# Kernel optimization log

Hardware: AMD Instinct MI355X
Metric: run time of the kernel (lower is better)

Reference implementation:

```python
import jax, jax.numpy as jnp
import numpy as np

# Mamba2 hyperparameters
D_MODEL = 768
D_STATE = 64
D_CONV = 4
EXPAND = 2
HEADDIM = 64
CHUNK = 64
D_INNER = EXPAND * D_MODEL            # 1536
NHEADS = D_INNER // HEADDIM           # 24
D_IN_PROJ = 2 * D_INNER + 2 * D_STATE + NHEADS  # 3224
CONV_DIM = D_INNER + 2 * D_STATE      # 1664
B_SZ = 8
SEQ = 4096  # multiple of CHUNK -> no padding branch


def setup_inputs() -> dict:
    key = jax.random.key(0)
    ks = jax.random.split(key, 6)
    u = jax.random.normal(ks[0], (B_SZ, SEQ, D_MODEL), jnp.float32)
    # fan-in scaled weights (matches nn.Linear/Conv1d default init scale)
    W_in = jax.random.normal(ks[1], (D_IN_PROJ, D_MODEL), jnp.float32) / np.sqrt(D_MODEL).astype(np.float32)
    conv_w = jax.random.normal(ks[2], (CONV_DIM, 1, D_CONV), jnp.float32) / np.sqrt(D_CONV).astype(np.float32)
    conv_b = jnp.zeros((CONV_DIM,), jnp.float32)
    dt_bias = jax.random.uniform(ks[3], (NHEADS,), jnp.float32, -4.0, 1.0)  # nn.init.uniform_(-4, 1)
    A_log = jnp.full((NHEADS,), -np.log(2.0), jnp.float32)                  # nn.init.constant_(-log 2)
    D_param = jnp.ones((NHEADS,), jnp.float32)
    norm_w = jnp.ones((D_INNER,), jnp.float32)
    W_out = jax.random.normal(ks[4], (D_MODEL, D_INNER), jnp.float32) / np.sqrt(D_INNER).astype(np.float32)
    return dict(u=u, W_in=W_in, conv_w=conv_w, conv_b=conv_b, dt_bias=dt_bias,
                A_log=A_log, D_param=D_param, norm_w=norm_w, W_out=W_out)


def _segsum(x):
    """Stable segment sum: out[..., i, j] = sum_{j < k <= i} x[..., k]; -inf above diagonal."""
    T = x.shape[-1]
    lower_strict = jnp.tril(jnp.ones((T, T), bool), -1)
    xe = jnp.where(lower_strict, x[..., :, None], 0.0)   # broadcast x over last (col) axis
    s = jnp.cumsum(xe, axis=-2)
    lower = jnp.tril(jnp.ones((T, T), bool), 0)
    return jnp.where(lower, s, -jnp.inf)


def _ssd(x, A, B, C, chunk):
    """Chunked SSD. x:(b,L,h,p)  A:(b,L,h)  B,C:(b,L,1,n)."""
    b, L, h, p = x.shape
    c = L // chunk
    n = B.shape[-1]
    x = x.reshape(b, c, chunk, h, p)
    A = A.reshape(b, c, chunk, h).transpose(0, 3, 1, 2)   # b h c l
    B = B.reshape(b, c, chunk, 1, n)
    C = C.reshape(b, c, chunk, 1, n)
    A_cs = jnp.cumsum(A, axis=-1)                          # b h c l
    # intra-chunk (diagonal) term
    Lmat = jnp.exp(_segsum(A))                             # b h c l s
    Y_diag = jnp.einsum('bclhn,bcshn,bhcls,bcshp->bclhp', C, B, Lmat, x)
    # per-chunk states
    decay_states = jnp.exp(A_cs[..., -1:] - A_cs)          # b h c l
    states = jnp.einsum('bclhn,bhcl,bclhp->bchpn', B, decay_states, x)
    states = jnp.concatenate([jnp.zeros_like(states[:, :1]), states], axis=1)  # b (c+1) h p n
    # inter-chunk recurrence
    A_last = jnp.pad(A_cs[..., -1], ((0, 0), (0, 0), (1, 0)))  # b h (c+1)
    decay_chunk = jnp.exp(_segsum(A_last))                     # b h (c+1) (c+1)
    new_states = jnp.einsum('bhzc,bchpn->bzhpn', decay_chunk, states)
    states = new_states[:, :-1]                                # b c h p n
    # off-diagonal (state-to-output) term
    Y_off = jnp.einsum('bclhn,bchpn,bhcl->bclhp', C, states, jnp.exp(A_cs))
    return (Y_diag + Y_off).reshape(b, L, h, p)


def reference(u, W_in, conv_w, conv_b, dt_bias, A_log, D_param, norm_w, W_out):
    b, L, _ = u.shape  # L % CHUNK == 0, so pad branch is a no-op
    zxbcdt = u @ W_in.T                                    # (b, L, D_IN_PROJ)
    z = zxbcdt[..., :D_INNER]
    xBC = zxbcdt[..., D_INNER:D_INNER + CONV_DIM]
    dt = jax.nn.softplus(zxbcdt[..., D_INNER + CONV_DIM:] + dt_bias)  # (b, L, h)
    # causal depthwise conv1d (torch pads both sides by d_conv-1 then slices [:L] == left pad)
    xBC = jax.lax.conv_general_dilated(
        xBC.transpose(0, 2, 1), conv_w, window_strides=(1,),
        padding=[(D_CONV - 1, 0)], dimension_numbers=('NCH', 'OIH', 'NCH'),
        feature_group_count=CONV_DIM)
    xBC = jax.nn.silu(xBC.transpose(0, 2, 1) + conv_b)     # (b, L, CONV_DIM)
    x = xBC[..., :D_INNER].reshape(b, L, NHEADS, HEADDIM)
    Bm = xBC[..., D_INNER:D_INNER + D_STATE][:, :, None, :]  # (b, L, 1, n)
    Cm = xBC[..., D_INNER + D_STATE:][:, :, None, :]
    A = -jnp.exp(A_log)                                    # (h,)
    Y = _ssd(x * dt[..., None], A * dt, Bm, Cm, CHUNK)
    y = Y + x * D_param[:, None]                           # skip term
    y = y.reshape(b, L, D_INNER)
    # gated RMSNorm: x * silu(z), then rmsnorm * weight
    y = y * jax.nn.silu(z)
    y = y * jax.lax.rsqrt(jnp.mean(y * y, axis=-1, keepdims=True) + 1e-5) * norm_w
    return y @ W_out.T
```

## Files before the change

### kernel.cpp

```cpp
#include <hip/hip_runtime.h>
#include <stdint.h>

typedef unsigned short u16;
typedef __bf16 bf16x8 __attribute__((ext_vector_type(8)));
typedef float f32x4 __attribute__((ext_vector_type(4)));
typedef unsigned short u16x8 __attribute__((ext_vector_type(8)));
typedef unsigned short u16x4 __attribute__((ext_vector_type(4)));
typedef __attribute__((address_space(1))) unsigned int gu32;
typedef __attribute__((address_space(3))) unsigned int lu32;

__device__ __forceinline__ float bf2f(u16 u){ unsigned int v=((unsigned int)u)<<16; float f; __builtin_memcpy(&f,&v,4); return f; }
__device__ __forceinline__ u16 f2bf(float f){ unsigned int v; __builtin_memcpy(&v,&f,4); v += 0x7fffu + ((v>>16)&1u); return (u16)(v>>16); }
__device__ __forceinline__ int swz(int r,int c){ return (r<<6) + (c ^ ((r&7)<<3)); }
__device__ __forceinline__ void glds16(const void* g, void* l){
  __builtin_amdgcn_global_load_lds((gu32*)g, (lu32*)l, 16, 0, 0);
}

__global__ __launch_bounds__(256) void k_cast(const float* __restrict__ in, u16* __restrict__ out, int n4){
  int i = blockIdx.x*256 + threadIdx.x;
  if (i >= n4) return;
  const f32x4 v = *(const f32x4*)(in + (size_t)i*4);
  u16x4 o; o.x=f2bf(v.x); o.y=f2bf(v.y); o.z=f2bf(v.z); o.w=f2bf(v.w);
  *(u16x4*)(out + (size_t)i*4) = o;
}

__global__ __launch_bounds__(256) void k_cast_pad(const float* __restrict__ in, u16* __restrict__ out){
  int i = blockIdx.x*256 + threadIdx.x;
  int e0 = i*4;
  int row = e0 / 768;
  int col = e0 - row*768;
  u16x4 o;
  if (row < 3224){
    const f32x4 v = *(const f32x4*)(in + (size_t)row*768 + col);
    o.x=f2bf(v.x); o.y=f2bf(v.y); o.z=f2bf(v.z); o.w=f2bf(v.w);
  } else { o.x=0; o.y=0; o.z=0; o.w=0; }
  *(u16x4*)(out + e0) = o;
}

template<int K, int NT, int EPI>
__global__ __launch_bounds__(256,4) void k_gemm(
    const u16* __restrict__ A, const u16* __restrict__ Bw,
    u16* __restrict__ o_z, u16* __restrict__ o_xbc, float* __restrict__ o_dt,
    const float* __restrict__ dt_bias, float* __restrict__ o_f32)
{
  __shared__ __align__(16) u16 Alds[8192];
  __shared__ __align__(16) u16 Blds[8192];
  const int tid = threadIdx.x;
  const int wave = tid>>6, lane = tid&63;
  const int nwg = gridDim.x;
  const int cpx = nwg>>3;
  const int bid = (int)blockIdx.x;
  const int sb  = (bid&7)*cpx + (bid>>3);
  const int m0 = (sb/NT)<<7, n0 = (sb%NT)<<7;
  const int wr = (wave>>1)<<6, wc = (wave&1)<<6;
  const int srow = tid>>3, sc0 = (tid&7)<<3;
  const int lo16 = lane&15, hi = lane>>4;
  f32x4 acc[4][4] = {};
  for (int k0 = 0; k0 < K; k0 += 64){
    #pragma unroll
    for (int i = 0; i < 4; ++i){
      const int row = (i<<5) + srow;
      const int scol = sc0 ^ ((row&7)<<3);
      glds16(A  + (size_t)(m0+row)*K + k0 + scol, &Alds[(i<<11) + (wave<<9)]);
      glds16(Bw + (size_t)(n0+row)*K + k0 + scol, &Blds[(i<<11) + (wave<<9)]);
    }
    __syncthreads();
    #pragma unroll
    for (int kk = 0; kk < 2; ++kk){
      const int kb = (kk<<5) + (hi<<3);
      bf16x8 af[4], bfv[4];
      #pragma unroll
      for (int m = 0; m < 4; ++m){
        const int r = wr + (m<<4) + lo16;
        af[m] = *(const bf16x8*)&Alds[(r<<6) + (kb ^ ((r&7)<<3))];
      }
      #pragma unroll
      for (int n = 0; n < 4; ++n){
        const int r = wc + (n<<4) + lo16;
        bfv[n] = *(const bf16x8*)&Blds[(r<<6) + (kb ^ ((r&7)<<3))];
      }
      #pragma unroll
      for (int m = 0; m < 4; ++m)
      #pragma unroll
      for (int n = 0; n < 4; ++n)
        acc[m][n] = __builtin_amdgcn_mfma_f32_16x16x32_bf16(af[m], bfv[n], acc[m][n], 0,0,0);
    }
    __syncthreads();
  }
  #pragma unroll
  for (int m = 0; m < 4; ++m)
  #pragma unroll
  for (int n = 0; n < 4; ++n)
  #pragma unroll
  for (int i = 0; i < 4; ++i){
    const int gr = m0 + wr + (m<<4) + (hi<<2) + i;
    const int gc = n0 + wc + (n<<4) + lo16;
    const float v = acc[m][n][i];
    if constexpr (EPI == 0){
      if (gc < 1536)      o_z[(size_t)gr*1536 + gc] = f2bf(v);
      else if (gc < 3200) o_xbc[(size_t)gr*1664 + (gc-1536)] = f2bf(v);
      else if (gc < 3224){
        const float t = v + dt_bias[gc-3200];
        o_dt[(size_t)(gc-3200)*32768 + gr] = (t > 20.f) ? t : log1pf(__expf(t));
      }
    } else {
      o_f32[(size_t)gr*768 + gc] = v;
    }
  }
}

__global__ __launch_bounds__(256) void k_conv(
    const u16* __restrict__ xbc, const float* __restrict__ cw, const float* __restrict__ cb,
    const float* __restrict__ dtT,
    u16* __restrict__ xT, u16* __restrict__ Bn, u16* __restrict__ BT, u16* __restrict__ Cn)
{
  const int idx = blockIdx.x*256 + threadIdx.x;
  if (idx >= 4096*208) return;
  const int g  = idx % 208;
  const int pt = idx / 208;
  const int ch0 = g << 3;
  const int m0 = pt << 3;
  const int l0 = m0 & 4095;
  float wgt[8][4], bias8[8];
  #pragma unroll
  for (int j = 0; j < 8; ++j){
    const f32x4 wv = *(const f32x4*)(cw + (size_t)(ch0+j)*4);
    wgt[j][0]=wv.x; wgt[j][1]=wv.y; wgt[j][2]=wv.z; wgt[j][3]=wv.w;
    bias8[j] = cb[ch0+j];
  }
  float acc[8][8];
  #pragma unroll
  for (int p = 0; p < 8; ++p)
  #pragma unroll
  for (int j = 0; j < 8; ++j) acc[p][j] = bias8[j];
  #pragma unroll
  for (int r = -3; r < 8; ++r){
    const int ls = l0 + r;
    if (ls < 0) continue;
    const u16x8 v = *(const u16x8*)(xbc + (size_t)(m0+r)*1664 + ch0);
    float xf[8];
    #pragma unroll
    for (int j = 0; j < 8; ++j) xf[j] = bf2f(v[j]);
    #pragma unroll
    for (int t = 0; t < 4; ++t){
      const int p = r + 3 - t;
      if (p < 0 || p > 7) continue;
      #pragma unroll
      for (int j = 0; j < 8; ++j) acc[p][j] += xf[j] * wgt[j][t];
    }
  }
  #pragma unroll
  for (int p = 0; p < 8; ++p)
  #pragma unroll
  for (int j = 0; j < 8; ++j){ const float s = acc[p][j]; acc[p][j] = s / (1.f + __expf(-s)); }

  const int b = m0 >> 12;
  const int cch = l0 >> 6;
  const int lr0 = l0 & 63;
  if (ch0 < 1536){
    const int h = ch0 >> 6, p0 = ch0 & 63;
    const f32x4 d0 = *(const f32x4*)(dtT + (size_t)h*32768 + m0);
    const f32x4 d1 = *(const f32x4*)(dtT + (size_t)h*32768 + m0 + 4);
    const float dtl[8] = {d0.x,d0.y,d0.z,d0.w,d1.x,d1.y,d1.z,d1.w};
    const size_t rb = (size_t)(b*24+h)*64;
    #pragma unroll
    for (int j = 0; j < 8; ++j){
      const int row = p0 + j;
      u16x8 o;
      #pragma unroll
      for (int p = 0; p < 8; ++p) o[p] = f2bf(acc[p][j] * dtl[p]);
      *(u16x8*)(xT + (rb + row)*4096 + (size_t)cch*64 + (lr0 ^ ((row&7)<<3))) = o;
    }
  } else if (ch0 < 1600){
    const int n0 = ch0 - 1536;
    const size_t tb = ((size_t)(b*64 + cch))*4096;
    #pragma unroll
    for (int p = 0; p < 8; ++p){
      const int lr = lr0 + p;
      u16x8 o;
      #pragma unroll
      for (int j = 0; j < 8; ++j) o[j] = f2bf(acc[p][j]);
      *(u16x8*)(Bn + tb + lr*64 + (n0 ^ ((lr&7)<<3))) = o;
    }
    #pragma unroll
    for (int j = 0; j < 8; ++j){
      const int row = n0 + j;
      u16x8 o;
      #pragma unroll
      for (int p = 0; p < 8; ++p) o[p] = f2bf(acc[p][j]);
      *(u16x8*)(BT + tb + row*64 + (lr0 ^ ((row&7)<<3))) = o;
    }
  } else {
    const int n0 = ch0 - 1600;
    const size_t tb = ((size_t)(b*64 + cch))*4096;
    #pragma unroll
    for (int p = 0; p < 8; ++p){
      const int lr = lr0 + p;
      u16x8 o;
      #pragma unroll
      for (int j = 0; j < 8; ++j) o[j] = f2bf(acc[p][j]);
      *(u16x8*)(Cn + tb + lr*64 + (n0 ^ ((lr&7)<<3))) = o;
    }
  }
}

__global__ __launch_bounds__(256,1) void k_ssd(
    const u16* __restrict__ xT, const u16* __restrict__ Bn, const u16* __restrict__ BT,
    const u16* __restrict__ Cn, const float* __restrict__ dtT, const float* __restrict__ A_log,
    const float* __restrict__ Dp, u16* __restrict__ yo)
{
  __shared__ __align__(16) u16 tiles[2][4][4096];
  __shared__ __align__(16) u16 Ml[4096];
  __shared__ __align__(16) u16 Sbf[4096];
  const int tid = threadIdx.x, wave = tid>>6, lane = tid&63;
  const int lo16 = lane&15, hi = lane>>4;
  const int w16 = wave<<4, hi4 = hi<<2;
  const int b = blockIdx.x / 24, h = blockIdx.x % 24;
  const float Ah = -__expf(A_log[h]);
  const float Dh = Dp[h];
  for (int i = tid; i < 4096; i += 256) Sbf[i] = 0;
  f32x4 Sreg[4] = {};
  const size_t xTg  = (size_t)(b*24+h)*64*4096;
  const size_t bcg  = (size_t)b*64*4096;
  const size_t dtg0 = (size_t)h*32768 + (size_t)b*4096;
  const size_t yb   = (size_t)b*4096*1536 + (size_t)h*64;

  auto stage = [&](int buf, int c){
    u16* dst = &tiles[buf][wave][0];
    if (wave == 0){
      const u16* g0 = xT + xTg + (size_t)c*64 + (size_t)(lane>>3)*4096 + (lane&7)*8;
      #pragma unroll
      for (int s = 0; s < 8; ++s) glds16(g0 + (size_t)s*32768, dst + s*512);
    } else {
      const u16* src = (wave==1 ? Bn : wave==2 ? BT : Cn) + bcg + (size_t)c*4096 + lane*8;
      #pragma unroll
      for (int s = 0; s < 8; ++s) glds16(src + s*512, dst + s*512);
    }
  };

  float dtc = dtT[dtg0 + lane];
  stage(0, 0);

  for (int c = 0; c < 64; ++c){
    float s = Ah * dtc;
    #pragma unroll
    for (int o = 1; o < 64; o <<= 1){ const float t = __shfl_up(s, o); if (lane >= o) s += t; }
    const float Alast = __shfl(s, 63);
    const float lam  = __expf(Alast);
    const float decl = __expf(Alast - s);
    const float elv  = __expf(s);
    float dtn = 0.f;
    if (c < 63){
      dtn = dtT[dtg0 + (size_t)(c+1)*64 + lane];
      stage((c+1)&1, c+1);
    }
    if (c == 0)       asm volatile("s_waitcnt vmcnt(9)  lgkmcnt(0)" ::: "memory");
    else if (c == 63) asm volatile("s_waitcnt vmcnt(4)  lgkmcnt(0)" ::: "memory");
    else              asm volatile("s_waitcnt vmcnt(13) lgkmcnt(0)" ::: "memory");
    __builtin_amdgcn_s_barrier();

    const u16* tx = &tiles[c&1][0][0];
    const u16* tb = &tiles[c&1][1][0];
    const u16* tt = &tiles[c&1][2][0];
    const u16* tc = &tiles[c&1][3][0];

    f32x4 accG[4] = {};
    bf16x8 bfC[2][4];
    #pragma unroll
    for (int kk = 0; kk < 2; ++kk){
      const int kb = (kk<<5) + (hi<<3);
      const int rA = w16 + lo16;
      const bf16x8 aB = *(const bf16x8*)&tb[(rA<<6) + (kb ^ ((rA&7)<<3))];
      #pragma unroll
      for (int t = 0; t < 4; ++t){
        const int rb = (t<<4) + lo16;
        bfC[kk][t] = *(const bf16x8*)&tc[(rb<<6) + (kb ^ ((rb&7)<<3))];
        accG[t] = __builtin_amdgcn_mfma_f32_16x16x32_bf16(aB, bfC[kk][t], accG[t], 0,0,0);
      }
    }
    float As_i[4];
    #pragma unroll
    for (int i = 0; i < 4; ++i) As_i[i] = __shfl(s, w16 + hi4 + i);
    #pragma unroll
    for (int t = 0; t < 4; ++t){
      const int l = (t<<4) + lo16;
      const float Al  = __shfl(s, l);
      const float dtl = __shfl(dtc, l);
      u16x4 ov;
      #pragma unroll
      for (int i = 0; i < 4; ++i){
        const int si = w16 + hi4 + i;
        float v = 0.f;
        if (si <= l) v = accG[t][i] * __expf(Al - As_i[i]);
        if (si == l) v += Dh / dtl;
        ov[i] = f2bf(v);
      }
      *(u16x4*)&Ml[(l<<6) + ((w16 + hi4) ^ ((l&7)<<3))] = ov;
    }
    asm volatile("s_waitcnt lgkmcnt(0)" ::: "memory");
    __builtin_amdgcn_s_barrier();

    f32x4 aYd[4] = {}, aYo[4] = {}, aS[4] = {};
    #pragma unroll
    for (int kk = 0; kk < 2; ++kk){
      const int kb = (kk<<5) + (hi<<3);
      const int rA = w16 + lo16;
      const int oA = (rA<<6) + (kb ^ ((rA&7)<<3));
      const bf16x8 aX = *(const bf16x8*)&tx[oA];
      const bf16x8 aSb= *(const bf16x8*)&Sbf[oA];
      const u16x8 aBTu= *(const u16x8*)&tt[oA];
      u16x8 aBTs;
      #pragma unroll
      for (int j = 0; j < 8; ++j) aBTs[j] = f2bf(bf2f(aBTu[j]) * __shfl(decl, kb + j));
      const bf16x8 aBT = *(const bf16x8*)&aBTs;
      #pragma unroll
      for (int t = 0; t < 4; ++t){
        const int rb = (t<<4) + lo16;
        const int o = (rb<<6) + (kb ^ ((rb&7)<<3));
        const bf16x8 bM = *(const bf16x8*)&Ml[o];
        const bf16x8 bX = *(const bf16x8*)&tx[o];
        aYd[t] = __builtin_amdgcn_mfma_f32_16x16x32_bf16(aX,  bM,         aYd[t], 0,0,0);
        aYo[t] = __builtin_amdgcn_mfma_f32_16x16x32_bf16(aSb, bfC[kk][t], aYo[t], 0,0,0);
        aS[t]  = __builtin_amdgcn_mfma_f32_16x16x32_bf16(aBT, bX,         aS[t],  0,0,0);
      }
    }
    asm volatile("s_waitcnt lgkmcnt(0)" ::: "memory");
    __builtin_amdgcn_s_barrier();

    #pragma unroll
    for (int t = 0; t < 4; ++t){
      const int p = (t<<4) + lo16;
      u16x4 sv;
      #pragma unroll
      for (int i = 0; i < 4; ++i){
        const float nv = Sreg[t][i] * lam + aS[t][i];
        Sreg[t][i] = nv;
        sv[i] = f2bf(nv);
      }
      *(u16x4*)&Sbf[(p<<6) + ((w16 + hi4) ^ ((p&7)<<3))] = sv;
    }
    #pragma unroll
    for (int t = 0; t < 4; ++t){
      const int l = (t<<4) + lo16;
      const float elt = __shfl(elv, l);
      u16x4 ov;
      #pragma unroll
      for (int i = 0; i < 4; ++i) ov[i] = f2bf(aYd[t][i] + elt * aYo[t][i]);
      *(u16x4*)(yo + yb + (size_t)((c<<6)+l)*1536 + w16 + hi4) = ov;
    }
    dtc = dtn;
  }
}

__global__ __launch_bounds__(192) void k_gnorm(
    const u16* __restrict__ y, const u16* __restrict__ z,
    const float* __restrict__ nw, u16* __restrict__ out)
{
  __shared__ float red[3];
  const int m = blockIdx.x, t = threadIdx.x;
  const size_t base = (size_t)m*1536 + t*8;
  const u16x8 yv = *(const u16x8*)(y + base);
  const u16x8 zv = *(const u16x8*)(z + base);
  float vals[8]; float ss = 0.f;
  #pragma unroll
  for (int j = 0; j < 8; ++j){
    const float zf = bf2f(zv[j]);
    const float v = bf2f(yv[j]) * zf / (1.f + __expf(-zf));
    vals[j] = v; ss += v*v;
  }
  #pragma unroll
  for (int off = 32; off > 0; off >>= 1) ss += __shfl_down(ss, off);
  if ((t & 63) == 0) red[t>>6] = ss;
  __syncthreads();
  const float sc = rsqrtf((red[0]+red[1]+red[2]) * (1.f/1536.f) + 1e-5f);
  u16x8 o;
  #pragma unroll
  for (int j = 0; j < 8; ++j) o[j] = f2bf(vals[j] * sc * nw[t*8+j]);
  *(u16x8*)(out + base) = o;
}

extern "C" void kernel_launch(void* const* d_in, const int* in_sizes, int n_in,
                              void* d_out, int out_size, void* d_ws, size_t ws_size,
                              hipStream_t stream)
{
  const float* u       = (const float*)d_in[0];
  const float* W_in    = (const float*)d_in[1];
  const float* conv_w  = (const float*)d_in[2];
  const float* conv_b  = (const float*)d_in[3];
  const float* dt_bias = (const float*)d_in[4];
  const float* A_log   = (const float*)d_in[5];
  const float* D_param = (const float*)d_in[6];
  const float* norm_w  = (const float*)d_in[7];
  const float* W_out   = (const float*)d_in[8];
  (void)in_sizes; (void)n_in; (void)out_size;
  if (ws_size < (size_t)379715584) return;

  char* w = (char*)d_ws;
  size_t off = 0;
  auto alloc = [&](size_t bytes)->void*{ void* p = w + off; off += (bytes + 255) & ~(size_t)255; return p; };
  u16* ubf    = (u16*)alloc(50331648);
  u16* winbf  = (u16*)alloc(5111808);
  u16* woutbf = (u16*)alloc(2359296);
  u16* zbf    = (u16*)alloc(100663296);
  u16* xbcbf  = (u16*)alloc(109051904);
  float* dtT  = (float*)alloc(3145728);
  u16* xTb    = (u16*)alloc(100663296);
  u16* Bnb    = (u16*)alloc(4194304);
  u16* Cnb    = (u16*)alloc(4194304);
  u16* BTb    = ubf;
  u16* yssd   = xbcbf;
  u16* ynorm  = xTb;

  k_cast<<<24576, 256, 0, stream>>>(u, ubf, 6291456);
  k_cast_pad<<<2496, 256, 0, stream>>>(W_in, winbf);
  k_cast<<<1152, 256, 0, stream>>>(W_out, woutbf, 294912);
  k_gemm<768,26,0><<<6656, 256, 0, stream>>>(ubf, winbf, zbf, xbcbf, dtT, dt_bias, nullptr);
  k_conv<<<3328, 256, 0, stream>>>(xbcbf, conv_w, conv_b, dtT, xTb, Bnb, BTb, Cnb);
  k_ssd<<<192, 256, 0, stream>>>(xTb, Bnb, BTb, Cnb, dtT, A_log, D_param, yssd);
  k_gnorm<<<32768, 192, 0, stream>>>(yssd, zbf, norm_w, ynorm);
  k_gemm<1536,6,1><<<1536, 256, 0, stream>>>(ynorm, woutbf, nullptr, nullptr, nullptr, nullptr, (float*)d_out);
}
```

Measured before the change: 689.3 us.

## Split SSD scan across headdim quarters to launch 4x more blocks

The SSD kernel previously ran one block per (batch, head), only 192 blocks on a GPU with far more CUs. It now splits the 64-wide head dimension into four 16-column slices, so 768 blocks each carry a quarter of the state and output. Launch bounds move to two blocks per CU and shared memory shrinks for the X and state tiles. The price is that every slice recomputes the C·B^T Gram matrix and the decay mask and reloads the full B and C tiles, adding redundant MFMA work and L2 traffic.

```diff
diff --git a/kernel.cpp b/kernel.cpp
--- a/kernel.cpp
+++ b/kernel.cpp
@@ -204,35 +204,39 @@
   }
 }
 
-__global__ __launch_bounds__(256,1) void k_ssd(
+__global__ __launch_bounds__(256,2) void k_ssd(
     const u16* __restrict__ xT, const u16* __restrict__ Bn, const u16* __restrict__ BT,
     const u16* __restrict__ Cn, const float* __restrict__ dtT, const float* __restrict__ A_log,
     const float* __restrict__ Dp, u16* __restrict__ yo)
 {
-  __shared__ __align__(16) u16 tiles[2][4][4096];
+  __shared__ __align__(16) u16 Xq[2][1024];
+  __shared__ __align__(16) u16 Bnl[2][4096];
+  __shared__ __align__(16) u16 BTl[2][4096];
+  __shared__ __align__(16) u16 Cnl[2][4096];
   __shared__ __align__(16) u16 Ml[4096];
-  __shared__ __align__(16) u16 Sbf[4096];
+  __shared__ __align__(16) u16 Sbf[1024];
   const int tid = threadIdx.x, wave = tid>>6, lane = tid&63;
   const int lo16 = lane&15, hi = lane>>4;
   const int w16 = wave<<4, hi4 = hi<<2;
-  const int b = blockIdx.x / 24, h = blockIdx.x % 24;
+  const int bid = (int)blockIdx.x;
+  const int b = bid / 96, rem = bid % 96, h = rem >> 2, p0 = (rem&3) << 4;
   const float Ah = -__expf(A_log[h]);
   const float Dh = Dp[h];
-  for (int i = tid; i < 4096; i += 256) Sbf[i] = 0;
-  f32x4 Sreg[4] = {};
+  for (int i = tid; i < 1024; i += 256) Sbf[i] = 0;
+  f32x4 Sreg = {};
   const size_t xTg  = (size_t)(b*24+h)*64*4096;
   const size_t bcg  = (size_t)b*64*4096;
   const size_t dtg0 = (size_t)h*32768 + (size_t)b*4096;
   const size_t yb   = (size_t)b*4096*1536 + (size_t)h*64;
 
   auto stage = [&](int buf, int c){
-    u16* dst = &tiles[buf][wave][0];
     if (wave == 0){
-      const u16* g0 = xT + xTg + (size_t)c*64 + (size_t)(lane>>3)*4096 + (lane&7)*8;
-      #pragma unroll
-      for (int s = 0; s < 8; ++s) glds16(g0 + (size_t)s*32768, dst + s*512);
+      const u16* g0 = xT + xTg + (size_t)c*64 + (size_t)(p0 + (lane>>3))*4096 + (lane&7)*8;
+      glds16(g0,               &Xq[buf][0]);
+      glds16(g0 + 8*4096,      &Xq[buf][512]);
     } else {
       const u16* src = (wave==1 ? Bn : wave==2 ? BT : Cn) + bcg + (size_t)c*4096 + lane*8;
+      u16* dst = (wave==1 ? &Bnl[buf][0] : wave==2 ? &BTl[buf][0] : &Cnl[buf][0]);
       #pragma unroll
       for (int s = 0; s < 8; ++s) glds16(src + s*512, dst + s*512);
     }
@@ -254,18 +258,23 @@
       dtn = dtT[dtg0 + (size_t)(c+1)*64 + lane];
       stage((c+1)&1, c+1);
     }
-    if (c == 0)       asm volatile("s_waitcnt vmcnt(9)  lgkmcnt(0)" ::: "memory");
-    else if (c == 63) asm volatile("s_waitcnt vmcnt(4)  lgkmcnt(0)" ::: "memory");
-    else              asm volatile("s_waitcnt vmcnt(13) lgkmcnt(0)" ::: "memory");
+    if (c == 0){
+      if (wave == 0) asm volatile("s_waitcnt vmcnt(2) lgkmcnt(0)" ::: "memory");
+      else           asm volatile("s_waitcnt vmcnt(8) lgkmcnt(0)" ::: "memory");
+    } else if (c == 63){
+      asm volatile("s_waitcnt vmcnt(0) lgkmcnt(0)" ::: "memory");
+    } else {
+      if (wave == 0) asm volatile("s_waitcnt vmcnt(3) lgkmcnt(0)" ::: "memory");
+      else           asm volatile("s_waitcnt vmcnt(9) lgkmcnt(0)" ::: "memory");
+    }
     __builtin_amdgcn_s_barrier();
 
-    const u16* tx = &tiles[c&1][0][0];
-    const u16* tb = &tiles[c&1][1][0];
-    const u16* tt = &tiles[c&1][2][0];
-    const u16* tc = &tiles[c&1][3][0];
+    const u16* tx = &Xq[c&1][0];
+    const u16* tb = &Bnl[c&1][0];
+    const u16* tt = &BTl[c&1][0];
+    const u16* tc = &Cnl[c&1][0];
 
     f32x4 accG[4] = {};
-    bf16x8 bfC[2][4];
     #pragma unroll
     for (int kk = 0; kk < 2; ++kk){
       const int kb = (kk<<5) + (hi<<3);
@@ -274,8 +283,8 @@
       #pragma unroll
       for (int t = 0; t < 4; ++t){
         const int rb = (t<<4) + lo16;
-        bfC[kk][t] = *(const bf16x8*)&tc[(rb<<6) + (kb ^ ((rb&7)<<3))];
-        accG[t] = __builtin_amdgcn_mfma_f32_16x16x32_bf16(aB, bfC[kk][t], accG[t], 0,0,0);
+        const bf16x8 bfC = *(const bf16x8*)&tc[(rb<<6) + (kb ^ ((rb&7)<<3))];
+        accG[t] = __builtin_amdgcn_mfma_f32_16x16x32_bf16(aB, bfC, accG[t], 0,0,0);
       }
     }
     float As_i[4];
@@ -300,53 +309,46 @@
     asm volatile("s_waitcnt lgkmcnt(0)" ::: "memory");
     __builtin_amdgcn_s_barrier();
 
-    f32x4 aYd[4] = {}, aYo[4] = {}, aS[4] = {};
+    f32x4 aYd = {}, aYo = {}, aS = {};
     #pragma unroll
     for (int kk = 0; kk < 2; ++kk){
       const int kb = (kk<<5) + (hi<<3);
-      const int rA = w16 + lo16;
-      const int oA = (rA<<6) + (kb ^ ((rA&7)<<3));
-      const bf16x8 aX = *(const bf16x8*)&tx[oA];
-      const bf16x8 aSb= *(const bf16x8*)&Sbf[oA];
-      const u16x8 aBTu= *(const u16x8*)&tt[oA];
+      const int oP = (lo16<<6) + (kb ^ ((lo16&7)<<3));
+      const int rW = w16 + lo16;
+      const int oW = (rW<<6) + (kb ^ ((rW&7)<<3));
+      const bf16x8 aX  = *(const bf16x8*)&tx[oP];
+      const bf16x8 aSb = *(const bf16x8*)&Sbf[oP];
+      const u16x8 aBTu = *(const u16x8*)&tt[oW];
       u16x8 aBTs;
       #pragma unroll
       for (int j = 0; j < 8; ++j) aBTs[j] = f2bf(bf2f(aBTu[j]) * __shfl(decl, kb + j));
       const bf16x8 aBT = *(const bf16x8*)&aBTs;
-      #pragma unroll
-      for (int t = 0; t < 4; ++t){
-        const int rb = (t<<4) + lo16;
-        const int o = (rb<<6) + (kb ^ ((rb&7)<<3));
-        const bf16x8 bM = *(const bf16x8*)&Ml[o];
-        const bf16x8 bX = *(const bf16x8*)&tx[o];
-        aYd[t] = __builtin_amdgcn_mfma_f32_16x16x32_bf16(aX,  bM,         aYd[t], 0,0,0);
-        aYo[t] = __builtin_amdgcn_mfma_f32_16x16x32_bf16(aSb, bfC[kk][t], aYo[t], 0,0,0);
-        aS[t]  = __builtin_amdgcn_mfma_f32_16x16x32_bf16(aBT, bX,         aS[t],  0,0,0);
-      }
+      const bf16x8 bM  = *(const bf16x8*)&Ml[oW];
+      const bf16x8 bC  = *(const bf16x8*)&tc[oW];
+      aYd = __builtin_amdgcn_mfma_f32_16x16x32_bf16(aX,  bM, aYd, 0,0,0);
+      aYo = __builtin_amdgcn_mfma_f32_16x16x32_bf16(aSb, bC, aYo, 0,0,0);
+      aS  = __builtin_amdgcn_mfma_f32_16x16x32_bf16(aBT, aX, aS,  0,0,0);
     }
     asm volatile("s_waitcnt lgkmcnt(0)" ::: "memory");
     __builtin_amdgcn_s_barrier();
 
-    #pragma unroll
-    for (int t = 0; t < 4; ++t){
-      const int p = (t<<4) + lo16;
+    {
       u16x4 sv;
       #pragma unroll
       for (int i = 0; i < 4; ++i){
-        const float nv = Sreg[t][i] * lam + aS[t][i];
-        Sreg[t][i] = nv;
+        const float nv = Sreg[i] * lam + aS[i];
+        Sreg[i] = nv;
         sv[i] = f2bf(nv);
       }
-      *(u16x4*)&Sbf[(p<<6) + ((w16 + hi4) ^ ((p&7)<<3))] = sv;
-    }
-    #pragma unroll
-    for (int t = 0; t < 4; ++t){
-      const int l = (t<<4) + lo16;
+      *(u16x4*)&Sbf[(lo16<<6) + ((w16 + hi4) ^ ((lo16&7)<<3))] = sv;
+    }
+    {
+      const int l = w16 + lo16;
       const float elt = __shfl(elv, l);
       u16x4 ov;
       #pragma unroll
-      for (int i = 0; i < 4; ++i) ov[i] = f2bf(aYd[t][i] + elt * aYo[t][i]);
-      *(u16x4*)(yo + yb + (size_t)((c<<6)+l)*1536 + w16 + hi4) = ov;
+      for (int i = 0; i < 4; ++i) ov[i] = f2bf(aYd[i] + elt * aYo[i]);
+      *(u16x4*)(yo + yb + (size_t)((c<<6)+l)*1536 + p0 + hi4) = ov;
     }
     dtc = dtn;
   }
@@ -416,7 +418,7 @@
   k_cast<<<1152, 256, 0, stream>>>(W_out, woutbf, 294912);
   k_gemm<768,26,0><<<6656, 256, 0, stream>>>(ubf, winbf, zbf, xbcbf, dtT, dt_bias, nullptr);
   k_conv<<<3328, 256, 0, stream>>>(xbcbf, conv_w, conv_b, dtT, xTb, Bnb, BTb, Cnb);
-  k_ssd<<<192, 256, 0, stream>>>(xTb, Bnb, BTb, Cnb, dtT, A_log, D_param, yssd);
+  k_ssd<<<768, 256, 0, stream>>>(xTb, Bnb, BTb, Cnb, dtT, A_log, D_param, yssd);
   k_gnorm<<<32768, 192, 0, stream>>>(yssd, zbf, norm_w, ynorm);
   k_gemm<1536,6,1><<<1536, 256, 0, stream>>>(ynorm, woutbf, nullptr, nullptr, nullptr, nullptr, (float*)d_out);
 }
```

After: 796.3 us. 15.5% more time.
